# Performance work log

Hardware: AMD Instinct MI355X
Metric: run time of the kernel (lower is better)

The kernel has to match this reference:

```python
import jax, jax.numpy as jnp
import numpy as np

OUT_SL = 32


def gru_cell(x, h, Wih, Whh, bih, bhh):
    # PyTorch GRU cell: gates ordered (r, z, n)
    gi = x @ Wih.T + bih
    gh = h @ Whh.T + bhh
    ir, iz, inn = jnp.split(gi, 3, axis=-1)
    hr, hz, hn = jnp.split(gh, 3, axis=-1)
    r = jax.nn.sigmoid(ir + hr)
    z = jax.nn.sigmoid(iz + hz)
    n = jnp.tanh(inn + r * hn)
    return (1.0 - z) * n + z * h


def run_gru_layer(xs, h0, Wih, Whh, bih, bhh, reverse=False):
    def step(h, x):
        h = gru_cell(x, h, Wih, Whh, bih, bhh)
        return h, h
    hT, ys = jax.lax.scan(step, h0, xs, reverse=reverse)
    return ys, hT


def setup_inputs() -> dict:
    key = jax.random.key(0)
    ks = iter(jax.random.split(key, 32))

    def p(shape, fan_in):
        return (jax.random.normal(next(ks), shape, dtype=jnp.float32)
                / np.sqrt(fan_in).astype(np.float32))

    V_ENC, V_DEC, EE, ED, NH = 32000, 32000, 300, 300, 256
    inp = jax.random.randint(next(ks), (128, 64), 0, V_ENC)
    return {
        'emb_enc': p((V_ENC, EE), 1.0),
        'enc_Wih0': p((2, 3 * NH, EE), EE),
        'enc_Whh0': p((2, 3 * NH, NH), NH),
        'enc_bih0': p((2, 3 * NH), NH),
        'enc_bhh0': p((2, 3 * NH), NH),
        'enc_Wih1': p((2, 3 * NH, 2 * NH), 2 * NH),
        'enc_Whh1': p((2, 3 * NH, NH), NH),
        'enc_bih1': p((2, 3 * NH), NH),
        'enc_bhh1': p((2, 3 * NH), NH),
        'W_out_enc': p((ED, 2 * NH), 2 * NH),
        'emb_dec': p((V_DEC, ED), 1.0),
        'dec_Wih': p((2, 3 * ED, ED), ED),
        'dec_Whh': p((2, 3 * ED, ED), ED),
        'dec_bih': p((2, 3 * ED), ED),
        'dec_bhh': p((2, 3 * ED), ED),
        'W1': p((2 * NH, ED), 2 * NH),
        'l2_W': p((ED, ED), ED),
        'l2_b': p((ED,), ED),
        'l3_W': p((ED, ED + 2 * NH), ED + 2 * NH),
        'l3_b': p((ED,), ED),
        'V_att': p((ED,), ED),
        'out_b': p((V_DEC,), ED),
        'inp': inp,
    }


def reference(emb_enc, enc_Wih0, enc_Whh0, enc_bih0, enc_bhh0,
              enc_Wih1, enc_Whh1, enc_bih1, enc_bhh1, W_out_enc,
              emb_dec, dec_Wih, dec_Whh, dec_bih, dec_bhh,
              W1, l2_W, l2_b, l3_W, l3_b, V_att, out_b, inp):
    sl, bs = inp.shape
    nh = enc_Whh0.shape[-1]
    h0 = jnp.zeros((bs, nh), dtype=emb_enc.dtype)

    # ---- encoder: 2-layer bidirectional GRU (dropout in eval mode = identity)
    emb = emb_enc[inp]                                        # (sl, bs, EE)
    yf0, hf0 = run_gru_layer(emb, h0, enc_Wih0[0], enc_Whh0[0], enc_bih0[0], enc_bhh0[0])
    yb0, hb0 = run_gru_layer(emb, h0, enc_Wih0[1], enc_Whh0[1], enc_bih0[1], enc_bhh0[1], reverse=True)
    x1 = jnp.concatenate([yf0, yb0], axis=-1)                 # (sl, bs, 2*nh)
    yf1, hf1 = run_gru_layer(x1, h0, enc_Wih1[0], enc_Whh1[0], enc_bih1[0], enc_bhh1[0])
    yb1, hb1 = run_gru_layer(x1, h0, enc_Wih1[1], enc_Whh1[1], enc_bih1[1], enc_bhh1[1], reverse=True)
    enc_out = jnp.concatenate([yf1, yb1], axis=-1)            # (sl, bs, 2*nh)

    # h.view(2,2,bs,-1).permute(0,2,1,3) -> concat fwd/bwd per layer
    h = jnp.stack([jnp.concatenate([hf0, hb0], axis=-1),
                   jnp.concatenate([hf1, hb1], axis=-1)])     # (2, bs, 2*nh)
    h = h @ W_out_enc.T                                       # (2, bs, ED)

    w1e = enc_out @ W1                                        # (sl, bs, ED)
    dec_inp0 = jnp.zeros((bs,), dtype=jnp.int32)

    def dec_step(carry, _):
        h, dec_inp = carry
        w2h = h[-1] @ l2_W.T + l2_b                           # (bs, ED)
        u = jnp.tanh(w1e + w2h[None])                         # (sl, bs, ED)
        a = jax.nn.softmax(u @ V_att, axis=0)                 # (sl, bs), softmax over seq
        Xa = jnp.einsum('sb,sbd->bd', a, enc_out)             # (bs, 2*nh)
        e = emb_dec[dec_inp]                                  # (bs, ED)
        x = jnp.concatenate([e, Xa], axis=1) @ l3_W.T + l3_b  # (bs, ED)
        h0n = gru_cell(x, h[0], dec_Wih[0], dec_Whh[0], dec_bih[0], dec_bhh[0])
        h1n = gru_cell(h0n, h[1], dec_Wih[1], dec_Whh[1], dec_bih[1], dec_bhh[1])
        outp = h1n @ emb_dec.T + out_b                        # (bs, V_dec), tied weights
        ndec = jnp.argmax(outp, axis=1).astype(jnp.int32)
        return (jnp.stack([h0n, h1n]), ndec), outp

    (_, _), res = jax.lax.scan(dec_step, (h, dec_inp0), None, length=OUT_SL)
    return res                                                # (out_sl, bs, V_dec)
```

## Files before the change

### kernel.cpp

```cpp
#include <hip/hip_runtime.h>
#include <math.h>


#define DINL static __device__ __forceinline__

DINL float sigm(float x) { return 1.0f / (1.0f + expf(-x)); }
DINL float dot4f(float4 a, float4 b) { return a.x*b.x + a.y*b.y + a.z*b.z + a.w*b.w; }

DINL unsigned long long packmax(float x, int v) {
  unsigned u = __float_as_uint(x);
  u = (u & 0x80000000u) ? ~u : (u | 0x80000000u);
  return ((unsigned long long)u << 32) | (unsigned)(~v);
}
DINL unsigned long long umax64(unsigned long long a, unsigned long long b) {
  return a > b ? a : b;
}

__global__ __launch_bounds__(256) void k_embed(const float4* __restrict__ E,
                                               const int* __restrict__ inp,
                                               float4* __restrict__ out) {
  int i = blockIdx.x * 256 + threadIdx.x;
  if (i >= 8192 * 75) return;
  int row = i / 75, q = i - row * 75;
  out[i] = E[(size_t)inp[row] * 75 + q];
}

__global__ __launch_bounds__(256) void k_transpose(const float* __restrict__ A,
                                                   float* __restrict__ B, int R, int C) {
  __shared__ float tile[32][33];
  int c0 = blockIdx.x * 32, r0 = blockIdx.y * 32;
  int tx = threadIdx.x & 31, ty = threadIdx.x >> 5;
  for (int i = 0; i < 32; i += 8) {
    int r = r0 + ty + i, c = c0 + tx;
    if (r < R && c < C) tile[ty + i][tx] = A[(size_t)r * C + c];
  }
  __syncthreads();
  for (int i = 0; i < 32; i += 8) {
    int c = c0 + ty + i, r = r0 + tx;
    if (c < C && r < R) B[(size_t)c * R + r] = tile[tx][ty + i];
  }
}

__global__ __launch_bounds__(256) void k_gemm128(const float* __restrict__ A,
                                                 const float* __restrict__ B,
                                                 const float* __restrict__ bias,
                                                 float* __restrict__ C,
                                                 int N, int M, int K) {
  __shared__ float As[8][132];
  __shared__ float Bs[8][132];
  const int tid = threadIdx.x;
  const int bn = blockIdx.x * 128, bm = blockIdx.y * 128;
  const int tn = (tid >> 4) << 3, tm = (tid & 15) << 3;
  const int r = tid & 127;
  const bool isB = tid >= 128;
  const float* src = isB ? (B + (size_t)(bm + r) * K) : (A + (size_t)(bn + r) * K);
  const bool rowok = isB ? (bm + r < M) : (bn + r < N);
  float acc[8][8] = {};
  for (int k0 = 0; k0 < K; k0 += 8) {
    float v[8];
    if (rowok && k0 + 8 <= K) {
      float4 p0 = *(const float4*)(src + k0);
      float4 p1 = *(const float4*)(src + k0 + 4);
      v[0]=p0.x; v[1]=p0.y; v[2]=p0.z; v[3]=p0.w;
      v[4]=p1.x; v[5]=p1.y; v[6]=p1.z; v[7]=p1.w;
    } else {
#pragma unroll
      for (int j = 0; j < 8; ++j) v[j] = (rowok && k0 + j < K) ? src[k0 + j] : 0.0f;
    }
    float (*dst)[132] = isB ? Bs : As;
#pragma unroll
    for (int j = 0; j < 8; ++j) dst[j][r] = v[j];
    __syncthreads();
#pragma unroll
    for (int kk = 0; kk < 8; ++kk) {
      float a[8], b[8];
      *(float4*)&a[0] = *(const float4*)&As[kk][tn];
      *(float4*)&a[4] = *(const float4*)&As[kk][tn + 4];
      *(float4*)&b[0] = *(const float4*)&Bs[kk][tm];
      *(float4*)&b[4] = *(const float4*)&Bs[kk][tm + 4];
#pragma unroll
      for (int i = 0; i < 8; ++i)
#pragma unroll
        for (int j = 0; j < 8; ++j) acc[i][j] += a[i] * b[j];
    }
    __syncthreads();
  }
#pragma unroll
  for (int i = 0; i < 8; ++i) {
    int row = bn + tn + i;
    if (row >= N) continue;
#pragma unroll
    for (int j = 0; j < 8; ++j) {
      int col = bm + tm + j;
      if (col < M) C[(size_t)row * M + col] = acc[i][j] + (bias ? bias[col] : 0.0f);
    }
  }
}

__global__ __launch_bounds__(256) void k_enc_layer(
    const float* __restrict__ giF, const float* __restrict__ giB,
    const float* __restrict__ Whh,
    const float* __restrict__ bhh,
    float* __restrict__ y,
    float* __restrict__ hbuf,
    int* __restrict__ bar) {
  const int dir = blockIdx.z;
  const int c0 = blockIdx.x * 16, b0 = blockIdx.y * 16;
  const int tid = threadIdx.x, cl = tid & 15, bl = tid >> 4;
  const float* gi = dir ? giB : giF;
  const float* W = Whh + (size_t)dir * 196608;
  const float* bh = bhh + dir * 768;
  float* hb = hbuf + dir * 16384;
  int* mybar = bar + (dir * 4 + blockIdx.y) * 128;

  __shared__ __align__(16) float Wlds[3][16][260];
  for (int i = tid; i < 48 * 64; i += 256) {
    int row = i >> 6, q = i & 63;
    int g = row >> 4, rc = row & 15;
    float4 w = ((const float4*)W)[(size_t)(c0 + rc + (g << 8)) * 64 + q];
    *(float4*)&Wlds[g][rc][q << 2] = w;
  }
  __syncthreads();

  const int b = b0 + bl, c = c0 + cl;
  const float bhr = bh[c], bhz = bh[256 + c], bhn = bh[512 + c];

  for (int t = 0; t < 128; ++t) {
    const int tt = dir ? 127 - t : t;
    const int pp = t & 1;
    const float* hrow = hb + pp * 32768 + (b << 8);
    float ar = 0.f, az = 0.f, an = 0.f;
#pragma unroll 4
    for (int k = 0; k < 256; k += 4) {
      float4 hv = *(const float4*)(hrow + k);
      float4 wr = *(const float4*)&Wlds[0][cl][k];
      float4 wz = *(const float4*)&Wlds[1][cl][k];
      float4 wn = *(const float4*)&Wlds[2][cl][k];
      ar += dot4f(hv, wr);
      az += dot4f(hv, wz);
      an += dot4f(hv, wn);
    }
    const float* gir = gi + (size_t)tt * 49152 + (size_t)b * 768;
    float rg = sigm(gir[c] + ar + bhr);
    float zg = sigm(gir[256 + c] + az + bhz);
    float ng = tanhf(gir[512 + c] + rg * (an + bhn));
    float hnew = (1.f - zg) * ng + zg * hrow[c];
    hb[(pp ^ 1) * 32768 + (b << 8) + c] = hnew;
    y[(size_t)tt * 32768 + (b << 9) + (dir << 8) + c] = hnew;

    if (t < 127) {
      __syncthreads();
      if (tid == 0) {
        __hip_atomic_fetch_add(&mybar[t], 1, __ATOMIC_RELEASE, __HIP_MEMORY_SCOPE_AGENT);
        while (__hip_atomic_load(&mybar[t], __ATOMIC_ACQUIRE, __HIP_MEMORY_SCOPE_AGENT) < 16)
          __builtin_amdgcn_s_sleep(1);
      }
      __syncthreads();
    }
  }
}

__global__ __launch_bounds__(256) void k_hcat(const float* __restrict__ x1,
                                              const float* __restrict__ encout,
                                              float* __restrict__ hcat) {
  int i = blockIdx.x * 256 + threadIdx.x;
  int l = i >> 15, r = i & 32767, b = r >> 9, d = r & 511;
  const float* src = l ? encout : x1;
  int ts = (d < 256) ? 127 : 0;
  hcat[i] = src[((size_t)(ts << 6) + b) * 512 + d];
}

__global__ __launch_bounds__(256) void k_dec_att(
    const float* __restrict__ h1, const float* __restrict__ w1e,
    const float* __restrict__ encout,
    const float* __restrict__ l2W, const float* __restrict__ l2b,
    const float* __restrict__ l3W, const float* __restrict__ l3b,
    const float* __restrict__ Vatt, const float* __restrict__ embdec,
    const unsigned long long* __restrict__ prev,
    float* __restrict__ xdec) {
  const int b = blockIdx.x, tid = threadIdx.x;
  __shared__ __align__(16) float h1s[300];
  __shared__ __align__(16) float w2h[300];
  __shared__ __align__(16) float eXa[812];
  __shared__ float aa[128];
  __shared__ float red[128];
  __shared__ unsigned long long redb[128];

  if (tid < 128) redb[tid] = (prev && tid < 125) ? prev[(size_t)tid * 64 + b] : 0ULL;
  for (int i = tid; i < 300; i += 256) h1s[i] = h1[b * 300 + i];
  __syncthreads();
  for (int s = 64; s > 0; s >>= 1) {
    if (tid < s) redb[tid] = umax64(redb[tid], redb[tid + s]);
    __syncthreads();
  }
  const int ib = prev ? (int)(~(unsigned)(redb[0] & 0xFFFFFFFFULL)) : 0;

  for (int m = tid; m < 300; m += 256) {
    const float4* wr = (const float4*)(l2W + (size_t)m * 300);
    const float4* hr = (const float4*)h1s;
    float acc = l2b[m];
    for (int q = 0; q < 75; ++q) acc += dot4f(wr[q], hr[q]);
    w2h[m] = acc;
  }
  __syncthreads();

  if (tid < 128) {
    const float4* wp = (const float4*)(w1e + ((size_t)(tid << 6) + b) * 300);
    const float4* vp = (const float4*)Vatt;
    const float4* hp = (const float4*)w2h;
    float acc = 0.f;
    for (int q = 0; q < 75; ++q) {
      float4 w = wp[q], h = hp[q], v = vp[q];
      acc += tanhf(w.x + h.x) * v.x + tanhf(w.y + h.y) * v.y +
             tanhf(w.z + h.z) * v.z + tanhf(w.w + h.w) * v.w;
    }
    aa[tid] = acc;
    red[tid] = acc;
  }
  __syncthreads();
  for (int s = 64; s > 0; s >>= 1) {
    if (tid < s) red[tid] = fmaxf(red[tid], red[tid + s]);
    __syncthreads();
  }
  float mx = red[0];
  __syncthreads();
  if (tid < 128) {
    float ex = expf(aa[tid] - mx);
    aa[tid] = ex;
    red[tid] = ex;
  }
  __syncthreads();
  for (int s = 64; s > 0; s >>= 1) {
    if (tid < s) red[tid] += red[tid + s];
    __syncthreads();
  }
  float inv = 1.0f / red[0];
  __syncthreads();
  if (tid < 128) aa[tid] *= inv;
  for (int d = tid; d < 300; d += 256) eXa[d] = embdec[(size_t)ib * 300 + d];
  __syncthreads();

  for (int d = tid; d < 512; d += 256) {
    float acc = 0.f;
    for (int s = 0; s < 128; ++s) acc += aa[s] * encout[((size_t)(s << 6) + b) * 512 + d];
    eXa[300 + d] = acc;
  }
  __syncthreads();

  for (int m = tid; m < 300; m += 256) {
    const float4* wr = (const float4*)(l3W + (size_t)m * 812);
    const float4* xr = (const float4*)eXa;
    float acc = l3b[m];
    for (int q = 0; q < 203; ++q) acc += dot4f(wr[q], xr[q]);
    xdec[b * 300 + m] = acc;
  }
}

__global__ __launch_bounds__(256) void k_gru300(
    const float* __restrict__ xin, const float* __restrict__ hin,
    float* __restrict__ hout, float* __restrict__ houtT,
    const float* __restrict__ Wih, const float* __restrict__ Whh,
    const float* __restrict__ bih, const float* __restrict__ bhh) {
  const int tid = threadIdx.x;
  const int cl = tid & 15, bl = tid >> 4;
  const int c = blockIdx.x * 16 + cl;
  const int b0 = blockIdx.y * 16;
  const int b = b0 + bl;
  __shared__ __align__(16) float xs[16][300];
  __shared__ __align__(16) float hs[16][300];
  for (int i = tid; i < 16 * 75; i += 256) {
    int row = i / 75, q = i - row * 75;
    ((float4*)&xs[row][0])[q] = ((const float4*)(xin + (size_t)(b0 + row) * 300))[q];
    ((float4*)&hs[row][0])[q] = ((const float4*)(hin + (size_t)(b0 + row) * 300))[q];
  }
  __syncthreads();
  if (c < 300) {
    float gir = bih[c], giz = bih[300 + c], gin = bih[600 + c];
    float ghr = bhh[c], ghz = bhh[300 + c], ghn = bhh[600 + c];
    const float4* wir = (const float4*)(Wih + (size_t)c * 300);
    const float4* wiz = (const float4*)(Wih + (size_t)(300 + c) * 300);
    const float4* win = (const float4*)(Wih + (size_t)(600 + c) * 300);
    const float4* whr = (const float4*)(Whh + (size_t)c * 300);
    const float4* whz = (const float4*)(Whh + (size_t)(300 + c) * 300);
    const float4* whn = (const float4*)(Whh + (size_t)(600 + c) * 300);
    const float4* xr = (const float4*)&xs[bl][0];
    const float4* hr = (const float4*)&hs[bl][0];
    for (int q = 0; q < 75; ++q) {
      float4 xv = xr[q], hv = hr[q];
      gir += dot4f(xv, wir[q]);
      giz += dot4f(xv, wiz[q]);
      gin += dot4f(xv, win[q]);
      ghr += dot4f(hv, whr[q]);
      ghz += dot4f(hv, whz[q]);
      ghn += dot4f(hv, whn[q]);
    }
    float r = sigm(gir + ghr), z = sigm(giz + ghz);
    float n = tanhf(gin + r * ghn);
    float hnew = (1.f - z) * n + z * hs[bl][c];
    hout[(size_t)b * 300 + c] = hnew;
    if (houtT) houtT[(size_t)c * 64 + b] = hnew;
  }
}

__global__ __launch_bounds__(256) void k_dec_out(const float* __restrict__ embT,
                                                 const float* __restrict__ h1T,
                                                 const float* __restrict__ outb,
                                                 float* __restrict__ out,
                                                 unsigned long long* __restrict__ bests) {
  const int tid = threadIdx.x;
  const int v = blockIdx.x * 256 + tid;
  const int bh = blockIdx.y;
  const float* h = h1T + bh * 32;
  __shared__ float accs[32][257];
  __shared__ unsigned long long red[256];
  float acc[32];
#pragma unroll
  for (int i = 0; i < 32; ++i) acc[i] = 0.f;
  for (int k = 0; k < 300; ++k) {
    float ev = embT[(size_t)k * 32000 + v];
#pragma unroll
    for (int i = 0; i < 32; ++i) acc[i] += ev * h[(size_t)k * 64 + i];
  }
  float bo = outb[v];
#pragma unroll
  for (int i = 0; i < 32; ++i) {
    float val = acc[i] + bo;
    out[(size_t)(bh * 32 + i) * 32000 + v] = val;
    accs[i][tid] = val;
  }
  __syncthreads();
  const int i2 = tid >> 3, j = tid & 7;
  unsigned long long best = 0ULL;
  for (int k = 0; k < 32; ++k) {
    int cc = (j << 5) | k;
    best = umax64(best, packmax(accs[i2][cc], (blockIdx.x << 8) | cc));
  }
  red[tid] = best;
  __syncthreads();
  if (tid < 32) {
    unsigned long long m = red[tid << 3];
#pragma unroll
    for (int k = 1; k < 8; ++k) m = umax64(m, red[(tid << 3) | k]);
    bests[(size_t)blockIdx.x * 64 + (bh << 5) + tid] = m;
  }
}

extern "C" void kernel_launch(void* const* d_in, const int* in_sizes, int n_in,
                              void* d_out_v, int out_size, void* d_ws, size_t ws_size,
                              hipStream_t stream) {
  (void)in_sizes; (void)n_in; (void)out_size; (void)ws_size;
  const float* emb_enc = (const float*)d_in[0];
  const float* eWih0   = (const float*)d_in[1];
  const float* eWhh0   = (const float*)d_in[2];
  const float* ebih0   = (const float*)d_in[3];
  const float* ebhh0   = (const float*)d_in[4];
  const float* eWih1   = (const float*)d_in[5];
  const float* eWhh1   = (const float*)d_in[6];
  const float* ebih1   = (const float*)d_in[7];
  const float* ebhh1   = (const float*)d_in[8];
  const float* Wout    = (const float*)d_in[9];
  const float* emb_dec = (const float*)d_in[10];
  const float* dWih    = (const float*)d_in[11];
  const float* dWhh    = (const float*)d_in[12];
  const float* dbih    = (const float*)d_in[13];
  const float* dbhh    = (const float*)d_in[14];
  const float* W1      = (const float*)d_in[15];
  const float* l2W     = (const float*)d_in[16];
  const float* l2b     = (const float*)d_in[17];
  const float* l3W     = (const float*)d_in[18];
  const float* l3b     = (const float*)d_in[19];
  const float* Vatt    = (const float*)d_in[20];
  const float* outb    = (const float*)d_in[21];
  const int* inp       = (const int*)d_in[22];
  float* d_out = (float*)d_out_v;

  float* ws = (float*)d_ws;
  size_t off = 0;
  auto take = [&](size_t n) { float* p = ws + off; off += (n + 3) & ~(size_t)3; return p; };
  float* embT   = take((size_t)300 * 32000);
  float* encout = take((size_t)8192 * 512);
  float* w1e    = take((size_t)8192 * 300);
  float* W1T    = take((size_t)300 * 512);
  float* hcat   = take((size_t)128 * 512);
  float* dech   = take((size_t)2 * 2 * 64 * 300);
  float* h1T    = take((size_t)300 * 64);
  float* xdec   = take((size_t)64 * 300);
  float* hbuf   = take((size_t)2 * 2 * 64 * 256);
  unsigned long long* bests = (unsigned long long*)take((size_t)125 * 64 * 2);
  int* bar      = (int*)take((size_t)2 * 8 * 128);

  float* emb  = d_out;
  float* gi0f = emb + 2457600;
  float* gi0b = gi0f + 6291456;
  float* x1   = gi0b + 6291456;
  float* gi1f = x1 + 4194304;
  float* gi1b = gi1f + 6291456;

  hipMemsetAsync(bar, 0, 2 * 8 * 128 * sizeof(int), stream);

  k_embed<<<2400, 256, 0, stream>>>((const float4*)emb_enc, inp, (float4*)emb);
  k_transpose<<<dim3(10, 16), 256, 0, stream>>>(W1, W1T, 512, 300);
  k_transpose<<<dim3(10, 1000), 256, 0, stream>>>(emb_dec, embT, 32000, 300);

  k_gemm128<<<dim3(64, 6), 256, 0, stream>>>(emb, eWih0, ebih0, gi0f, 8192, 768, 300);
  k_gemm128<<<dim3(64, 6), 256, 0, stream>>>(emb, eWih0 + 230400, ebih0 + 768, gi0b, 8192, 768, 300);
  hipMemsetAsync(hbuf, 0, 2 * 2 * 64 * 256 * sizeof(float), stream);
  k_enc_layer<<<dim3(16, 4, 2), 256, 0, stream>>>(gi0f, gi0b, eWhh0, ebhh0, x1, hbuf, bar);

  k_gemm128<<<dim3(64, 6), 256, 0, stream>>>(x1, eWih1, ebih1, gi1f, 8192, 768, 512);
  k_gemm128<<<dim3(64, 6), 256, 0, stream>>>(x1, eWih1 + 393216, ebih1 + 768, gi1b, 8192, 768, 512);
  hipMemsetAsync(hbuf, 0, 2 * 2 * 64 * 256 * sizeof(float), stream);
  k_enc_layer<<<dim3(16, 4, 2), 256, 0, stream>>>(gi1f, gi1b, eWhh1, ebhh1, encout, hbuf, bar + 1024);

  k_hcat<<<256, 256, 0, stream>>>(x1, encout, hcat);
  k_gemm128<<<dim3(1, 3), 256, 0, stream>>>(hcat, Wout, nullptr, dech, 128, 300, 512);
  k_gemm128<<<dim3(64, 3), 256, 0, stream>>>(encout, W1T, nullptr, w1e, 8192, 300, 512);

  for (int t = 0; t < 32; ++t) {
    int cur = t & 1, nxt = cur ^ 1;
    float* hc = dech + cur * 38400;
    float* hn = dech + nxt * 38400;
    k_dec_att<<<64, 256, 0, stream>>>(hc + 19200, w1e, encout, l2W, l2b, l3W, l3b,
                                      Vatt, emb_dec, t ? bests : nullptr, xdec);
    k_gru300<<<dim3(19, 4), 256, 0, stream>>>(xdec, hc, hn, nullptr,
                                              dWih, dWhh, dbih, dbhh);
    k_gru300<<<dim3(19, 4), 256, 0, stream>>>(hn, hc + 19200, hn + 19200, h1T,
                                              dWih + 270000, dWhh + 270000,
                                              dbih + 900, dbhh + 900);
    k_dec_out<<<dim3(125, 2), 256, 0, stream>>>(embT, h1T, outb,
                                                d_out + (size_t)t * 2048000, bests);
  }
}
```

Before: 10.34 ms.

## Fuse decoder step kernels with flag barriers and rework encoder recurrence split

The encoder recurrence now uses 8-batch blocks (doubling the grid), stages h into shared memory, splits the K reduction across thread pairs with shuffles, prefetches the next step's input gates, and replaces the counter barrier with per-block flag barriers. The decoder fuses attention and both GRU cells into one persistent 76-block kernel synchronised by grid flag barriers, saving two launches per step. The output projection now computes all 64 batch rows per block with a split-K over two thread halves, changing the argmax partial layout to 250 blocks. This trades launch overhead and barrier contention for spin-wait barriers that require all blocks to be co-resident, plus higher register pressure in the output kernel.

```diff
diff --git a/kernel.cpp b/kernel.cpp
--- a/kernel.cpp
+++ b/kernel.cpp
@@ -14,6 +14,17 @@
 }
 DINL unsigned long long umax64(unsigned long long a, unsigned long long b) {
   return a > b ? a : b;
+}
+
+DINL void flagbar(int* flags, int selfid, int n, int target, int tid) {
+  __syncthreads();
+  if (tid == 0)
+    __hip_atomic_store(&flags[selfid * 32], target, __ATOMIC_RELEASE, __HIP_MEMORY_SCOPE_AGENT);
+  for (int i = tid; i < n; i += 256) {
+    while (__hip_atomic_load(&flags[i * 32], __ATOMIC_ACQUIRE, __HIP_MEMORY_SCOPE_AGENT) < target)
+      __builtin_amdgcn_s_sleep(1);
+  }
+  __syncthreads();
 }
 
 __global__ __launch_bounds__(256) void k_embed(const float4* __restrict__ E,
@@ -103,59 +114,88 @@
     const float* __restrict__ bhh,
     float* __restrict__ y,
     float* __restrict__ hbuf,
-    int* __restrict__ bar) {
+    int* __restrict__ flags) {
   const int dir = blockIdx.z;
-  const int c0 = blockIdx.x * 16, b0 = blockIdx.y * 16;
-  const int tid = threadIdx.x, cl = tid & 15, bl = tid >> 4;
+  const int c0 = blockIdx.x << 4;
+  const int b0 = blockIdx.y << 3;
+  const int tid = threadIdx.x;
+  const int cl = tid >> 4;
+  const int bl = (tid >> 1) & 7;
+  const int ks = tid & 1;
   const float* gi = dir ? giB : giF;
   const float* W = Whh + (size_t)dir * 196608;
   const float* bh = bhh + dir * 768;
   float* hb = hbuf + dir * 16384;
-  int* mybar = bar + (dir * 4 + blockIdx.y) * 128;
-
-  __shared__ __align__(16) float Wlds[3][16][260];
+  int* myflags = flags + ((dir << 3) + blockIdx.y) * 16 * 32;
+
+  __shared__ __align__(16) float W0[16][260], W1[16][260], W2[16][260];
+  __shared__ __align__(16) float hsh[8][260];
+
   for (int i = tid; i < 48 * 64; i += 256) {
     int row = i >> 6, q = i & 63;
     int g = row >> 4, rc = row & 15;
     float4 w = ((const float4*)W)[(size_t)(c0 + rc + (g << 8)) * 64 + q];
-    *(float4*)&Wlds[g][rc][q << 2] = w;
+    float* dst = (g == 0) ? &W0[rc][0] : ((g == 1) ? &W1[rc][0] : &W2[rc][0]);
+    *(float4*)&dst[q << 2] = w;
   }
   __syncthreads();
 
   const int b = b0 + bl, c = c0 + cl;
   const float bhr = bh[c], bhz = bh[256 + c], bhn = bh[512 + c];
-
-  for (int t = 0; t < 128; ++t) {
-    const int tt = dir ? 127 - t : t;
-    const int pp = t & 1;
-    const float* hrow = hb + pp * 32768 + (b << 8);
-    float ar = 0.f, az = 0.f, an = 0.f;
-#pragma unroll 4
-    for (int k = 0; k < 256; k += 4) {
-      float4 hv = *(const float4*)(hrow + k);
-      float4 wr = *(const float4*)&Wlds[0][cl][k];
-      float4 wz = *(const float4*)&Wlds[1][cl][k];
-      float4 wn = *(const float4*)&Wlds[2][cl][k];
-      ar += dot4f(hv, wr);
-      az += dot4f(hv, wz);
-      an += dot4f(hv, wn);
-    }
-    const float* gir = gi + (size_t)tt * 49152 + (size_t)b * 768;
-    float rg = sigm(gir[c] + ar + bhr);
-    float zg = sigm(gir[256 + c] + az + bhz);
-    float ng = tanhf(gir[512 + c] + rg * (an + bhn));
-    float hnew = (1.f - zg) * ng + zg * hrow[c];
-    hb[(pp ^ 1) * 32768 + (b << 8) + c] = hnew;
-    y[(size_t)tt * 32768 + (b << 9) + (dir << 8) + c] = hnew;
-
-    if (t < 127) {
+  const int kbase = ks << 7;
+
+  {
+    const int tt0 = dir ? 127 : 0;
+    const float* gp = gi + (size_t)tt0 * 49152 + (size_t)b * 768;
+    float gr0 = gp[c], gz0 = gp[256 + c], gn0 = gp[512 + c];
+    float gr = gr0, gz = gz0, gn = gn0;
+
+    for (int t = 0; t < 128; ++t) {
+      const int pp = t & 1;
+      {
+        const float* hsrc = hb + pp * 32768 + (b0 << 8);
+        int i0 = tid, b1 = i0 >> 6, k1 = i0 & 63;
+        int i1 = tid + 256, b2 = i1 >> 6, k2 = i1 & 63;
+        float4 h0 = *(const float4*)(hsrc + (b1 << 8) + (k1 << 2));
+        float4 h1 = *(const float4*)(hsrc + (b2 << 8) + (k2 << 2));
+        *(float4*)&hsh[b1][k1 << 2] = h0;
+        *(float4*)&hsh[b2][k2 << 2] = h1;
+      }
       __syncthreads();
-      if (tid == 0) {
-        __hip_atomic_fetch_add(&mybar[t], 1, __ATOMIC_RELEASE, __HIP_MEMORY_SCOPE_AGENT);
-        while (__hip_atomic_load(&mybar[t], __ATOMIC_ACQUIRE, __HIP_MEMORY_SCOPE_AGENT) < 16)
-          __builtin_amdgcn_s_sleep(1);
-      }
-      __syncthreads();
+
+      float nr = 0.f, nz = 0.f, nn = 0.f;
+      if (t < 127) {
+        const int tn_ = dir ? 126 - t : t + 1;
+        const float* gp2 = gi + (size_t)tn_ * 49152 + (size_t)b * 768;
+        nr = gp2[c]; nz = gp2[256 + c]; nn = gp2[512 + c];
+      }
+
+      float ar = 0.f, az = 0.f, an = 0.f;
+#pragma unroll 8
+      for (int kq = 0; kq < 32; ++kq) {
+        const int k = kbase + (kq << 2);
+        float4 hv = *(const float4*)&hsh[bl][k];
+        ar += dot4f(hv, *(const float4*)&W0[cl][k]);
+        az += dot4f(hv, *(const float4*)&W1[cl][k]);
+        an += dot4f(hv, *(const float4*)&W2[cl][k]);
+      }
+      ar += __shfl_xor(ar, 1);
+      az += __shfl_xor(az, 1);
+      an += __shfl_xor(an, 1);
+
+      float rg = sigm(gr + ar + bhr);
+      float zg = sigm(gz + az + bhz);
+      float ng = tanhf(gn + rg * (an + bhn));
+      float hnew = (1.f - zg) * ng + zg * hsh[bl][c];
+
+      if (ks == 0) {
+        const int tt = dir ? 127 - t : t;
+        hb[(pp ^ 1) * 32768 + (b << 8) + c] = hnew;
+        y[(size_t)tt * 32768 + (b << 9) + (dir << 8) + c] = hnew;
+      }
+      gr = nr; gz = nz; gn = nn;
+
+      if (t < 127) flagbar(myflags, blockIdx.x, 16, t + 1, tid);
     }
   }
 }
@@ -170,108 +210,20 @@
   hcat[i] = src[((size_t)(ts << 6) + b) * 512 + d];
 }
 
-__global__ __launch_bounds__(256) void k_dec_att(
-    const float* __restrict__ h1, const float* __restrict__ w1e,
-    const float* __restrict__ encout,
-    const float* __restrict__ l2W, const float* __restrict__ l2b,
-    const float* __restrict__ l3W, const float* __restrict__ l3b,
-    const float* __restrict__ Vatt, const float* __restrict__ embdec,
-    const unsigned long long* __restrict__ prev,
-    float* __restrict__ xdec) {
-  const int b = blockIdx.x, tid = threadIdx.x;
-  __shared__ __align__(16) float h1s[300];
-  __shared__ __align__(16) float w2h[300];
-  __shared__ __align__(16) float eXa[812];
-  __shared__ float aa[128];
-  __shared__ float red[128];
-  __shared__ unsigned long long redb[128];
-
-  if (tid < 128) redb[tid] = (prev && tid < 125) ? prev[(size_t)tid * 64 + b] : 0ULL;
-  for (int i = tid; i < 300; i += 256) h1s[i] = h1[b * 300 + i];
-  __syncthreads();
-  for (int s = 64; s > 0; s >>= 1) {
-    if (tid < s) redb[tid] = umax64(redb[tid], redb[tid + s]);
-    __syncthreads();
-  }
-  const int ib = prev ? (int)(~(unsigned)(redb[0] & 0xFFFFFFFFULL)) : 0;
-
-  for (int m = tid; m < 300; m += 256) {
-    const float4* wr = (const float4*)(l2W + (size_t)m * 300);
-    const float4* hr = (const float4*)h1s;
-    float acc = l2b[m];
-    for (int q = 0; q < 75; ++q) acc += dot4f(wr[q], hr[q]);
-    w2h[m] = acc;
-  }
-  __syncthreads();
-
-  if (tid < 128) {
-    const float4* wp = (const float4*)(w1e + ((size_t)(tid << 6) + b) * 300);
-    const float4* vp = (const float4*)Vatt;
-    const float4* hp = (const float4*)w2h;
-    float acc = 0.f;
-    for (int q = 0; q < 75; ++q) {
-      float4 w = wp[q], h = hp[q], v = vp[q];
-      acc += tanhf(w.x + h.x) * v.x + tanhf(w.y + h.y) * v.y +
-             tanhf(w.z + h.z) * v.z + tanhf(w.w + h.w) * v.w;
-    }
-    aa[tid] = acc;
-    red[tid] = acc;
-  }
-  __syncthreads();
-  for (int s = 64; s > 0; s >>= 1) {
-    if (tid < s) red[tid] = fmaxf(red[tid], red[tid + s]);
-    __syncthreads();
-  }
-  float mx = red[0];
-  __syncthreads();
-  if (tid < 128) {
-    float ex = expf(aa[tid] - mx);
-    aa[tid] = ex;
-    red[tid] = ex;
-  }
-  __syncthreads();
-  for (int s = 64; s > 0; s >>= 1) {
-    if (tid < s) red[tid] += red[tid + s];
-    __syncthreads();
-  }
-  float inv = 1.0f / red[0];
-  __syncthreads();
-  if (tid < 128) aa[tid] *= inv;
-  for (int d = tid; d < 300; d += 256) eXa[d] = embdec[(size_t)ib * 300 + d];
-  __syncthreads();
-
-  for (int d = tid; d < 512; d += 256) {
-    float acc = 0.f;
-    for (int s = 0; s < 128; ++s) acc += aa[s] * encout[((size_t)(s << 6) + b) * 512 + d];
-    eXa[300 + d] = acc;
-  }
-  __syncthreads();
-
-  for (int m = tid; m < 300; m += 256) {
-    const float4* wr = (const float4*)(l3W + (size_t)m * 812);
-    const float4* xr = (const float4*)eXa;
-    float acc = l3b[m];
-    for (int q = 0; q < 203; ++q) acc += dot4f(wr[q], xr[q]);
-    xdec[b * 300 + m] = acc;
-  }
-}
-
-__global__ __launch_bounds__(256) void k_gru300(
-    const float* __restrict__ xin, const float* __restrict__ hin,
-    float* __restrict__ hout, float* __restrict__ houtT,
-    const float* __restrict__ Wih, const float* __restrict__ Whh,
-    const float* __restrict__ bih, const float* __restrict__ bhh) {
-  const int tid = threadIdx.x;
+DINL void gru_phase(int cb, int tid, const float* __restrict__ xin,
+                    const float* __restrict__ hin, float* __restrict__ hout,
+                    float* __restrict__ houtT,
+                    const float* __restrict__ Wih, const float* __restrict__ Whh,
+                    const float* __restrict__ bih, const float* __restrict__ bhh,
+                    float* xs, float* hs) {
+  const int cchunk = cb % 19, bchunk = cb / 19;
   const int cl = tid & 15, bl = tid >> 4;
-  const int c = blockIdx.x * 16 + cl;
-  const int b0 = blockIdx.y * 16;
-  const int b = b0 + bl;
-  __shared__ __align__(16) float xs[16][300];
-  __shared__ __align__(16) float hs[16][300];
+  const int c = cchunk * 16 + cl;
+  const int b0 = bchunk * 16, bq = b0 + bl;
   for (int i = tid; i < 16 * 75; i += 256) {
     int row = i / 75, q = i - row * 75;
-    ((float4*)&xs[row][0])[q] = ((const float4*)(xin + (size_t)(b0 + row) * 300))[q];
-    ((float4*)&hs[row][0])[q] = ((const float4*)(hin + (size_t)(b0 + row) * 300))[q];
+    ((float4*)(xs + row * 300))[q] = ((const float4*)(xin + (size_t)(b0 + row) * 300))[q];
+    ((float4*)(hs + row * 300))[q] = ((const float4*)(hin + (size_t)(b0 + row) * 300))[q];
   }
   __syncthreads();
   if (c < 300) {
@@ -283,8 +235,8 @@
     const float4* whr = (const float4*)(Whh + (size_t)c * 300);
     const float4* whz = (const float4*)(Whh + (size_t)(300 + c) * 300);
     const float4* whn = (const float4*)(Whh + (size_t)(600 + c) * 300);
-    const float4* xr = (const float4*)&xs[bl][0];
-    const float4* hr = (const float4*)&hs[bl][0];
+    const float4* xr = (const float4*)(xs + bl * 300);
+    const float4* hr = (const float4*)(hs + bl * 300);
     for (int q = 0; q < 75; ++q) {
       float4 xv = xr[q], hv = hr[q];
       gir += dot4f(xv, wir[q]);
@@ -296,10 +248,118 @@
     }
     float r = sigm(gir + ghr), z = sigm(giz + ghz);
     float n = tanhf(gin + r * ghn);
-    float hnew = (1.f - z) * n + z * hs[bl][c];
-    hout[(size_t)b * 300 + c] = hnew;
-    if (houtT) houtT[(size_t)c * 64 + b] = hnew;
-  }
+    float hnew = (1.f - z) * n + z * hs[bl * 300 + c];
+    hout[(size_t)bq * 300 + c] = hnew;
+    if (houtT) houtT[(size_t)c * 64 + bq] = hnew;
+  }
+}
+
+__global__ __launch_bounds__(256) void k_dec_step(
+    const float* __restrict__ hc, float* __restrict__ hn, float* __restrict__ h1T,
+    const float* __restrict__ w1e, const float* __restrict__ encout,
+    const float* __restrict__ l2W, const float* __restrict__ l2b,
+    const float* __restrict__ l3W, const float* __restrict__ l3b,
+    const float* __restrict__ Vatt, const float* __restrict__ embdec,
+    const float* __restrict__ dWih, const float* __restrict__ dWhh,
+    const float* __restrict__ dbih, const float* __restrict__ dbhh,
+    const unsigned long long* __restrict__ prev,
+    float* __restrict__ xdec, int* __restrict__ flags, int tstep) {
+  const int tid = threadIdx.x, cb = blockIdx.x;
+  __shared__ __align__(16) float smem[9600];
+  float* h1s = smem;
+  float* w2h = smem + 304;
+  float* eXa = smem + 608;
+  float* aa  = smem + 1424;
+  float* red = smem + 1552;
+  unsigned long long* redb = (unsigned long long*)(smem + 1680);
+
+  if (cb < 64) {
+    const int b = cb;
+    const float* h1 = hc + 19200;
+    if (tid < 128) {
+      unsigned long long m = 0ULL;
+      if (prev) {
+        m = prev[(size_t)tid * 64 + b];
+        if (tid < 122) m = umax64(m, prev[(size_t)(tid + 128) * 64 + b]);
+      }
+      redb[tid] = m;
+    }
+    for (int i = tid; i < 300; i += 256) h1s[i] = h1[b * 300 + i];
+    __syncthreads();
+    for (int s = 64; s > 0; s >>= 1) {
+      if (tid < s) redb[tid] = umax64(redb[tid], redb[tid + s]);
+      __syncthreads();
+    }
+    const int ib = prev ? (int)(~(unsigned)(redb[0] & 0xFFFFFFFFULL)) : 0;
+
+    for (int m = tid; m < 300; m += 256) {
+      const float4* wr = (const float4*)(l2W + (size_t)m * 300);
+      const float4* hr = (const float4*)h1s;
+      float acc = l2b[m];
+      for (int q = 0; q < 75; ++q) acc += dot4f(wr[q], hr[q]);
+      w2h[m] = acc;
+    }
+    __syncthreads();
+
+    if (tid < 128) {
+      const float4* wp = (const float4*)(w1e + ((size_t)(tid << 6) + b) * 300);
+      const float4* vp = (const float4*)Vatt;
+      const float4* hp = (const float4*)w2h;
+      float acc = 0.f;
+      for (int q = 0; q < 75; ++q) {
+        float4 w = wp[q], h = hp[q], v = vp[q];
+        acc += tanhf(w.x + h.x) * v.x + tanhf(w.y + h.y) * v.y +
+               tanhf(w.z + h.z) * v.z + tanhf(w.w + h.w) * v.w;
+      }
+      aa[tid] = acc;
+      red[tid] = acc;
+    }
+    __syncthreads();
+    for (int s = 64; s > 0; s >>= 1) {
+      if (tid < s) red[tid] = fmaxf(red[tid], red[tid + s]);
+      __syncthreads();
+    }
+    float mx = red[0];
+    __syncthreads();
+    if (tid < 128) {
+      float ex = expf(aa[tid] - mx);
+      aa[tid] = ex;
+      red[tid] = ex;
+    }
+    __syncthreads();
+    for (int s = 64; s > 0; s >>= 1) {
+      if (tid < s) red[tid] += red[tid + s];
+      __syncthreads();
+    }
+    float inv = 1.0f / red[0];
+    __syncthreads();
+    if (tid < 128) aa[tid] *= inv;
+    for (int d = tid; d < 300; d += 256) eXa[d] = embdec[(size_t)ib * 300 + d];
+    __syncthreads();
+
+    for (int d = tid; d < 512; d += 256) {
+      float acc = 0.f;
+      for (int s = 0; s < 128; ++s) acc += aa[s] * encout[((size_t)(s << 6) + b) * 512 + d];
+      eXa[300 + d] = acc;
+    }
+    __syncthreads();
+
+    for (int m = tid; m < 300; m += 256) {
+      const float4* wr = (const float4*)(l3W + (size_t)m * 812);
+      const float4* xr = (const float4*)eXa;
+      float acc = l3b[m];
+      for (int q = 0; q < 203; ++q) acc += dot4f(wr[q], xr[q]);
+      xdec[b * 300 + m] = acc;
+    }
+  }
+
+  flagbar(flags, cb, 76, 2 * tstep + 1, tid);
+  gru_phase(cb, tid, xdec, hc, hn, nullptr, dWih, dWhh, dbih, dbhh,
+            smem, smem + 4800);
+  flagbar(flags, cb, 76, 2 * tstep + 2, tid);
+  gru_phase(cb, tid, hn, hc + 19200, hn + 19200, h1T,
+            dWih + 270000, dWhh + 270000, dbih + 900, dbhh + 900,
+            smem, smem + 4800);
 }
 
 __global__ __launch_bounds__(256) void k_dec_out(const float* __restrict__ embT,
@@ -308,40 +368,40 @@
                                                  float* __restrict__ out,
                                                  unsigned long long* __restrict__ bests) {
   const int tid = threadIdx.x;
-  const int v = blockIdx.x * 256 + tid;
-  const int bh = blockIdx.y;
-  const float* h = h1T + bh * 32;
-  __shared__ float accs[32][257];
-  __shared__ unsigned long long red[256];
-  float acc[32];
-#pragma unroll
-  for (int i = 0; i < 32; ++i) acc[i] = 0.f;
-  for (int k = 0; k < 300; ++k) {
+  const int vt = tid & 127, kh = tid >> 7;
+  const int v = blockIdx.x * 128 + vt;
+  __shared__ float sacc[128][65];
+  float acc[64];
+#pragma unroll
+  for (int i = 0; i < 64; ++i) acc[i] = 0.f;
+  const int kb = kh * 150;
+  for (int k = kb; k < kb + 150; ++k) {
     float ev = embT[(size_t)k * 32000 + v];
-#pragma unroll
-    for (int i = 0; i < 32; ++i) acc[i] += ev * h[(size_t)k * 64 + i];
-  }
-  float bo = outb[v];
-#pragma unroll
-  for (int i = 0; i < 32; ++i) {
-    float val = acc[i] + bo;
-    out[(size_t)(bh * 32 + i) * 32000 + v] = val;
-    accs[i][tid] = val;
-  }
-  __syncthreads();
-  const int i2 = tid >> 3, j = tid & 7;
-  unsigned long long best = 0ULL;
-  for (int k = 0; k < 32; ++k) {
-    int cc = (j << 5) | k;
-    best = umax64(best, packmax(accs[i2][cc], (blockIdx.x << 8) | cc));
-  }
-  red[tid] = best;
-  __syncthreads();
-  if (tid < 32) {
-    unsigned long long m = red[tid << 3];
-#pragma unroll
-    for (int k = 1; k < 8; ++k) m = umax64(m, red[(tid << 3) | k]);
-    bests[(size_t)blockIdx.x * 64 + (bh << 5) + tid] = m;
+    const float* h = h1T + k * 64;
+#pragma unroll
+    for (int i = 0; i < 64; ++i) acc[i] += ev * h[i];
+  }
+  if (kh) {
+#pragma unroll
+    for (int i = 0; i < 64; ++i) sacc[vt][i] = acc[i];
+  }
+  __syncthreads();
+  if (!kh) {
+    float bo = outb[v];
+#pragma unroll
+    for (int i = 0; i < 64; ++i) {
+      float val = acc[i] + sacc[vt][i] + bo;
+      out[(size_t)i * 32000 + v] = val;
+      sacc[vt][i] = val;
+    }
+  }
+  __syncthreads();
+  if (tid < 64) {
+    unsigned long long best = 0ULL;
+    const int v0 = blockIdx.x * 128;
+    for (int q = 0; q < 128; ++q)
+      best = umax64(best, packmax(sacc[q][tid], v0 + q));
+    bests[(size_t)blockIdx.x * 64 + tid] = best;
   }
 }
 
@@ -386,8 +446,9 @@
   float* h1T    = take((size_t)300 * 64);
   float* xdec   = take((size_t)64 * 300);
   float* hbuf   = take((size_t)2 * 2 * 64 * 256);
-  unsigned long long* bests = (unsigned long long*)take((size_t)125 * 64 * 2);
-  int* bar      = (int*)take((size_t)2 * 8 * 128);
+  unsigned long long* bests = (unsigned long long*)take((size_t)250 * 64 * 2);
+  int* flags_enc = (int*)take((size_t)2 * 16 * 16 * 32);
+  int* flags_dec = (int*)take((size_t)76 * 32);
 
   float* emb  = d_out;
   float* gi0f = emb + 2457600;
@@ -396,7 +457,7 @@
   float* gi1f = x1 + 4194304;
   float* gi1b = gi1f + 6291456;
 
-  hipMemsetAsync(bar, 0, 2 * 8 * 128 * sizeof(int), stream);
+  hipMemsetAsync(flags_enc, 0, (2 * 16 * 16 * 32 + 76 * 32) * sizeof(int), stream);
 
   k_embed<<<2400, 256, 0, stream>>>((const float4*)emb_enc, inp, (float4*)emb);
   k_transpose<<<dim3(10, 16), 256, 0, stream>>>(W1, W1T, 512, 300);
@@ -405,12 +466,13 @@
   k_gemm128<<<dim3(64, 6), 256, 0, stream>>>(emb, eWih0, ebih0, gi0f, 8192, 768, 300);
   k_gemm128<<<dim3(64, 6), 256, 0, stream>>>(emb, eWih0 + 230400, ebih0 + 768, gi0b, 8192, 768, 300);
   hipMemsetAsync(hbuf, 0, 2 * 2 * 64 * 256 * sizeof(float), stream);
-  k_enc_layer<<<dim3(16, 4, 2), 256, 0, stream>>>(gi0f, gi0b, eWhh0, ebhh0, x1, hbuf, bar);
+  k_enc_layer<<<dim3(16, 8, 2), 256, 0, stream>>>(gi0f, gi0b, eWhh0, ebhh0, x1, hbuf, flags_enc);
 
   k_gemm128<<<dim3(64, 6), 256, 0, stream>>>(x1, eWih1, ebih1, gi1f, 8192, 768, 512);
   k_gemm128<<<dim3(64, 6), 256, 0, stream>>>(x1, eWih1 + 393216, ebih1 + 768, gi1b, 8192, 768, 512);
   hipMemsetAsync(hbuf, 0, 2 * 2 * 64 * 256 * sizeof(float), stream);
-  k_enc_layer<<<dim3(16, 4, 2), 256, 0, stream>>>(gi1f, gi1b, eWhh1, ebhh1, encout, hbuf, bar + 1024);
+  k_enc_layer<<<dim3(16, 8, 2), 256, 0, stream>>>(gi1f, gi1b, eWhh1, ebhh1, encout, hbuf,
+                                                  flags_enc + 8192);
 
   k_hcat<<<256, 256, 0, stream>>>(x1, encout, hcat);
   k_gemm128<<<dim3(1, 3), 256, 0, stream>>>(hcat, Wout, nullptr, dech, 128, 300, 512);
@@ -420,14 +482,10 @@
     int cur = t & 1, nxt = cur ^ 1;
     float* hc = dech + cur * 38400;
     float* hn = dech + nxt * 38400;
-    k_dec_att<<<64, 256, 0, stream>>>(hc + 19200, w1e, encout, l2W, l2b, l3W, l3b,
-                                      Vatt, emb_dec, t ? bests : nullptr, xdec);
-    k_gru300<<<dim3(19, 4), 256, 0, stream>>>(xdec, hc, hn, nullptr,
-                                              dWih, dWhh, dbih, dbhh);
-    k_gru300<<<dim3(19, 4), 256, 0, stream>>>(hn, hc + 19200, hn + 19200, h1T,
-                                              dWih + 270000, dWhh + 270000,
-                                              dbih + 900, dbhh + 900);
-    k_dec_out<<<dim3(125, 2), 256, 0, stream>>>(embT, h1T, outb,
-                                                d_out + (size_t)t * 2048000, bests);
-  }
-}
+    k_dec_step<<<76, 256, 0, stream>>>(hc, hn, h1T, w1e, encout, l2W, l2b, l3W, l3b,
+                                       Vatt, emb_dec, dWih, dWhh, dbih, dbhh,
+                                       t ? bests : nullptr, xdec, flags_dec, t);
+    k_dec_out<<<250, 256, 0, stream>>>(embT, h1T, outb,
+                                       d_out + (size_t)t * 2048000, bests);
+  }
+}
```

New measurement: 12.83 ms. +24.0%, slower.
